# Kernel optimization log

Measured on AMD Instinct MI355X. Metric: run time of the kernel, lower is better.

## Reference

```python
import jax, jax.numpy as jnp
import numpy as np

B, S, D, V, T, NS, NG = 16, 512, 400, 32000, 8, 30, 3


def setup_inputs() -> dict:
    key = jax.random.key(0)
    ks = jax.random.split(key, 14)
    w = 1.0 / np.sqrt(D)
    return {
        "encoded_hidden": jax.random.normal(ks[0], (1, B, D), jnp.float32) * 0.1,
        "encoded_outputs": jax.random.normal(ks[1], (B, S, D), jnp.float32) * 0.1,
        "story": jax.random.randint(ks[2], (B, S), 0, V),
        "trg_batches": jax.random.randint(ks[3], (B, NS, T), 0, V),
        "shared_emb": jax.random.normal(ks[4], (V, D), jnp.float32) * 0.1,
        "slot_emb": jax.random.normal(ks[5], (1, D), jnp.float32) * 0.1,
        "w_ih": jax.random.normal(ks[6], (3 * D, D), jnp.float32) * w,
        "w_hh": jax.random.normal(ks[7], (3 * D, D), jnp.float32) * w,
        "b_ih": jax.random.normal(ks[8], (3 * D,), jnp.float32) * w,
        "b_hh": jax.random.normal(ks[9], (3 * D,), jnp.float32) * w,
        "w_ratio_w": jax.random.normal(ks[10], (1, 3 * D), jnp.float32) * w,
        "w_ratio_b": jax.random.normal(ks[11], (1,), jnp.float32) * w,
        "w_gate_w": jax.random.normal(ks[12], (NG, D), jnp.float32) * w,
        "w_gate_b": jax.random.normal(ks[13], (NG,), jnp.float32) * w,
        "batch_size": B,
        "max_resp_len": T,
    }


def reference(encoded_hidden, encoded_outputs, story, trg_batches, shared_emb,
              slot_emb, w_ih, w_hh, b_ih, b_hh, w_ratio_w, w_ratio_b,
              w_gate_w, w_gate_b, batch_size, max_resp_len):
    # Original torch code returns inside the slot loop -> only slot 0 is decoded.
    # h0 is re-used as GRU initial state at EVERY step (no carried hidden), and
    # teacher forcing makes each step's input known, so all T steps vectorize.
    h0 = encoded_hidden[0]                         # (B, D)
    Bq, Tq = batch_size, max_resp_len
    Vq = shared_emb.shape[0]

    # decoder inputs: step 0 = slot embedding, steps 1..T-1 = emb(trg[:,0,i-1])
    x0 = jnp.broadcast_to(slot_emb, h0.shape)      # (B, D)
    xt = shared_emb[trg_batches[:, 0, : Tq - 1]]   # (B, T-1, D)
    X = jnp.concatenate([x0[:, None, :], xt], axis=1)  # (B, T, D)

    # GRU cell (torch gate order r, z, n), h0 broadcast over steps
    gi = X @ w_ih.T + b_ih                         # (B, T, 3D)
    gh = h0 @ w_hh.T + b_hh                        # (B, 3D)
    i_r, i_z, i_n = jnp.split(gi, 3, axis=-1)
    h_r, h_z, h_n = jnp.split(gh, 3, axis=-1)
    r = jax.nn.sigmoid(i_r + h_r[:, None, :])
    z = jax.nn.sigmoid(i_z + h_z[:, None, :])
    n = jnp.tanh(i_n + r * h_n[:, None, :])
    h = (1.0 - z) * n + z * h0[:, None, :]         # (B, T, D) decoder_state == hidden

    # attention over history (no length masking: all lens == S)
    scores = jnp.einsum('btd,bsd->bts', h, encoded_outputs)   # (B, T, S)
    probs = jax.nn.softmax(scores, axis=-1)
    # FAITHFUL to original bug: context uses raw scores, not probs
    context = jnp.einsum('bts,bsd->btd', scores, encoded_outputs)

    gate0 = context[:, 0, :] @ w_gate_w.T + w_gate_b          # (B, NG), step i==0

    p_vocab = jax.nn.softmax(h @ shared_emb.T, axis=-1)       # (B, T, V)
    p_gen = jax.nn.sigmoid(
        jnp.concatenate([h, context, X], axis=-1) @ w_ratio_w.T + w_ratio_b
    )                                                         # (B, T, 1)

    # pointer distribution: scatter_add probs onto vocab ids of the story
    p_ctx = jnp.zeros((Bq, Tq, Vq), p_vocab.dtype).at[
        jnp.arange(Bq)[:, None, None],
        jnp.arange(Tq)[None, :, None],
        story[:, None, :],
    ].add(probs)

    p_final = p_gen * p_vocab + (1.0 - p_gen) * p_ctx         # (B, T, V)

    ptr_outputs = jnp.zeros((NS, Bq, Tq, Vq), p_final.dtype).at[0].set(p_final)
    gate_outputs = jnp.zeros((NS, Bq, NG), gate0.dtype).at[0].set(gate0)
    return ptr_outputs, gate_outputs
```

## Files before the change

kernel.cpp:

```cpp
#include <hip/hip_runtime.h>

#define Bq 16
#define Sq 512
#define Dq 400
#define Vq 32000
#define Tq 8
#define NSq 30
#define NGq 3
#define BTq (Bq*Tq)
#define SLICE 4096000
#define PTR_TOTAL (30ull*SLICE)
#define GATE_TOTAL (NSq*Bq*NGq)

#define NCOMPUTE 250
#define NZERO 1813
#define ZPER 16384

#define GCOMPUTE 64
#define PCTX_ZB 250

__device__ inline float sigmoidf_(float x) { return 1.0f / (1.0f + __expf(-x)); }

__device__ inline float blockReduceSum(float v, float* red) {
    int tid = threadIdx.x;
    #pragma unroll
    for (int o = 32; o > 0; o >>= 1) v += __shfl_down(v, o, 64);
    if ((tid & 63) == 0) red[tid >> 6] = v;
    __syncthreads();
    if (tid == 0) {
        float s = red[0];
        int nw = blockDim.x >> 6;
        for (int i = 1; i < nw; i++) s += red[i];
        red[0] = s;
    }
    __syncthreads();
    float r = red[0];
    __syncthreads();
    return r;
}

__device__ inline float blockReduceMax(float v, float* red) {
    int tid = threadIdx.x;
    #pragma unroll
    for (int o = 32; o > 0; o >>= 1) v = fmaxf(v, __shfl_down(v, o, 64));
    if ((tid & 63) == 0) red[tid >> 6] = v;
    __syncthreads();
    if (tid == 0) {
        float s = red[0];
        int nw = blockDim.x >> 6;
        for (int i = 1; i < nw; i++) s = fmaxf(s, red[i]);
        red[0] = s;
    }
    __syncthreads();
    float r = red[0];
    __syncthreads();
    return r;
}

__global__ __launch_bounds__(256) void k_gates(const float* __restrict__ enc_hidden,
                                               const float* __restrict__ shared_emb,
                                               const float* __restrict__ slot_emb,
                                               const float* __restrict__ w_ih,
                                               const float* __restrict__ w_hh,
                                               const float* __restrict__ b_ih,
                                               const float* __restrict__ b_hh,
                                               const int* __restrict__ trg,
                                               float* __restrict__ gi, float* __restrict__ gh,
                                               float* __restrict__ pctx) {
    int tid = threadIdx.x;
    if (blockIdx.x >= GCOMPUTE) {
        int zb = blockIdx.x - GCOMPUTE;
        float4 z = make_float4(0.0f, 0.0f, 0.0f, 0.0f);
        float4* dst = (float4*)pctx;
        size_t base = (size_t)zb * 4096 + tid;
        #pragma unroll
        for (int r = 0; r < 16; ++r) dst[base + (size_t)r * 256] = z;
        return;
    }
    __shared__ float A[9][Dq];
    __shared__ int toks[8];
    int b = blockIdx.x >> 2, jt = blockIdx.x & 3;
    if (tid < 7) toks[tid + 1] = trg[b * (NSq * Tq) + tid];
    __syncthreads();
    for (int idx = tid; idx < 900; idx += 256) {
        int r = idx / 100, q = idx - r * 100;
        const float4* src;
        if (r == 8)      src = (const float4*)(enc_hidden + b * Dq);
        else if (r == 0) src = (const float4*)slot_emb;
        else             src = (const float4*)(shared_emb + (size_t)toks[r] * Dq);
        *(float4*)&A[r][4 * q] = src[q];
    }
    __syncthreads();
    for (int o = tid; o < 2700; o += 256) {
        int r = o / 300, jj = o - r * 300;
        int j = jt * 300 + jj;
        const float* w = (r == 8) ? w_hh : w_ih;
        const float4* w4 = (const float4*)(w + (size_t)j * Dq);
        const float4* a4 = (const float4*)&A[r][0];
        float acc = (r == 8) ? b_hh[j] : b_ih[j];
        #pragma unroll 4
        for (int q = 0; q < Dq / 4; ++q) {
            float4 wv = w4[q], av = a4[q];
            acc += av.x * wv.x + av.y * wv.y + av.z * wv.z + av.w * wv.w;
        }
        if (r == 8) gh[b * 1200 + j] = acc;
        else        gi[(b * 8 + r) * 1200 + j] = acc;
    }
}

__global__ __launch_bounds__(512) void k_attn(const float* __restrict__ gi,
                                              const float* __restrict__ gh,
                                              const float* __restrict__ enc_hidden,
                                              const float* __restrict__ shared_emb,
                                              const float* __restrict__ slot_emb,
                                              const int* __restrict__ trg,
                                              const float* __restrict__ enc_out,
                                              const int* __restrict__ story,
                                              const float* __restrict__ w_ratio_w,
                                              const float* __restrict__ w_ratio_b,
                                              const float* __restrict__ w_gate_w,
                                              const float* __restrict__ w_gate_b,
                                              float* __restrict__ pctx, float* __restrict__ pgen,
                                              float* __restrict__ hT, float* __restrict__ out_gate) {
    __shared__ float h_l[Dq], ctx_l[Dq], x_l[Dq], sc_l[Sq], red[8];
    int bt = blockIdx.x, b = bt >> 3, t = bt & 7;
    int tid = threadIdx.x;
    if (tid < Dq) {
        int d = tid;
        float x = (t == 0) ? slot_emb[d]
                           : shared_emb[(size_t)trg[b * (NSq * Tq) + (t - 1)] * Dq + d];
        float h0 = enc_hidden[b * Dq + d];
        const float* gib = gi + bt * 1200;
        const float* ghb = gh + b * 1200;
        float r_ = sigmoidf_(gib[d] + ghb[d]);
        float z  = sigmoidf_(gib[Dq + d] + ghb[Dq + d]);
        float n  = tanhf(gib[2 * Dq + d] + r_ * ghb[2 * Dq + d]);
        float h  = (1.0f - z) * n + z * h0;
        h_l[d] = h; x_l[d] = x;
        hT[d * BTq + bt] = h;
    }
    __syncthreads();
    {
        const float4* e4 = (const float4*)(enc_out + ((size_t)(b * Sq + tid)) * Dq);
        float acc = 0.0f;
        for (int q = 0; q < Dq / 4; ++q) {
            float4 p = e4[q];
            int k = 4 * q;
            acc += h_l[k]*p.x + h_l[k+1]*p.y + h_l[k+2]*p.z + h_l[k+3]*p.w;
        }
        sc_l[tid] = acc;
    }
    __syncthreads();
    float myv = sc_l[tid];
    float m = blockReduceMax(myv, red);
    float e = __expf(myv - m);
    float ssum = blockReduceSum(e, red);
    atomicAdd(&pctx[(size_t)bt * Vq + story[b * Sq + tid]], e / ssum);
    for (int d = tid; d < Dq; d += 512) {
        float acc = 0.0f;
        #pragma unroll 8
        for (int s = 0; s < Sq; ++s)
            acc += sc_l[s] * enc_out[((size_t)(b * Sq + s)) * Dq + d];
        ctx_l[d] = acc;
    }
    __syncthreads();
    {
        float part = 0.0f;
        for (int i = tid; i < 1200; i += 512) {
            float v = (i < Dq) ? h_l[i] : (i < 2 * Dq ? ctx_l[i - Dq] : x_l[i - 2 * Dq]);
            part += v * w_ratio_w[i];
        }
        float tot = blockReduceSum(part, red);
        if (tid == 0) pgen[bt] = sigmoidf_(tot + w_ratio_b[0]);
    }
    if (t == 0) {
        for (int g = 0; g < NGq; ++g) {
            float part = 0.0f;
            for (int d = tid; d < Dq; d += 512) part += ctx_l[d] * w_gate_w[g * Dq + d];
            float tot = blockReduceSum(part, red);
            if (tid == 0) out_gate[b * NGq + g] = tot + w_gate_b[g];
        }
    }
}

#define TVL 128
#define CKL 40
__global__ __launch_bounds__(256) void k_logits(const float* __restrict__ hT,
                                                const float* __restrict__ emb,
                                                float* __restrict__ logits,
                                                float* __restrict__ out) {
    __shared__ float eT[CKL][132];
    __shared__ float hL[CKL][132];
    int bid = blockIdx.x;
    int tid = threadIdx.x;
    if (bid >= NCOMPUTE) {
        int zb = bid - NCOMPUTE;
        float4 z = make_float4(0.0f, 0.0f, 0.0f, 0.0f);
        if (zb < NZERO) {
            float4* dst = (float4*)(out + (size_t)SLICE);
            const size_t total = 29ull * SLICE / 4;
            size_t base = (size_t)zb * ZPER + tid;
            #pragma unroll
            for (int r = 0; r < ZPER / 256; ++r) {
                size_t idx = base + (size_t)r * 256;
                if (idx < total) dst[idx] = z;
            }
        } else {
            float4* g = (float4*)(out + PTR_TOTAL + Bq * NGq);
            for (int i = tid; i < (GATE_TOTAL - Bq * NGq) / 4; i += 256) g[i] = z;
        }
        return;
    }
    int v0 = bid * TVL;
    int tx = tid & 15, ty = tid >> 4;
    float acc[8][8];
    #pragma unroll
    for (int j = 0; j < 8; ++j)
        #pragma unroll
        for (int i = 0; i < 8; ++i) acc[j][i] = 0.0f;

    for (int c = 0; c < Dq / CKL; ++c) {
        int k0 = c * CKL;
        const float4* hg = (const float4*)(hT + (size_t)k0 * BTq);
        #pragma unroll
        for (int r = 0; r < 5; ++r) {
            int idx = tid + 256 * r;
            int k = idx >> 5, c4 = idx & 31;
            float4 vd = hg[idx];
            *(float4*)&hL[k][4 * c4] = vd;
        }
        #pragma unroll
        for (int r = 0; r < 5; ++r) {
            int idx = tid + 256 * r;
            int v = idx / 10, q = idx - 10 * v;
            float4 vd = *(const float4*)(emb + (size_t)(v0 + v) * Dq + k0 + 4 * q);
            eT[4*q+0][v] = vd.x; eT[4*q+1][v] = vd.y; eT[4*q+2][v] = vd.z; eT[4*q+3][v] = vd.w;
        }
        __syncthreads();
        #pragma unroll 4
        for (int k = 0; k < CKL; ++k) {
            float4 h0 = *(const float4*)&hL[k][8 * ty];
            float4 h1 = *(const float4*)&hL[k][8 * ty + 4];
            float4 e0 = *(const float4*)&eT[k][8 * tx];
            float4 e1 = *(const float4*)&eT[k][8 * tx + 4];
            float hv[8] = {h0.x, h0.y, h0.z, h0.w, h1.x, h1.y, h1.z, h1.w};
            float ev[8] = {e0.x, e0.y, e0.z, e0.w, e1.x, e1.y, e1.z, e1.w};
            #pragma unroll
            for (int j = 0; j < 8; ++j)
                #pragma unroll
                for (int i = 0; i < 8; ++i)
                    acc[j][i] += hv[j] * ev[i];
        }
        __syncthreads();
    }
    #pragma unroll
    for (int j = 0; j < 8; ++j) {
        int bt = 8 * ty + j;
        float* dst = logits + (size_t)bt * Vq + v0 + 8 * tx;
        *(float4*)dst       = make_float4(acc[j][0], acc[j][1], acc[j][2], acc[j][3]);
        *(float4*)(dst + 4) = make_float4(acc[j][4], acc[j][5], acc[j][6], acc[j][7]);
    }
}

__global__ __launch_bounds__(512) void k_final(const float* __restrict__ logits,
                                               const float* __restrict__ pctx,
                                               const float* __restrict__ pgen,
                                               float* __restrict__ out) {
    __shared__ float red[8];
    int bt = blockIdx.x, tid = threadIdx.x;
    const float* lr = logits + (size_t)bt * Vq;
    float m = -1e30f;
    for (int v = tid; v < Vq; v += 512) m = fmaxf(m, lr[v]);
    m = blockReduceMax(m, red);
    float s = 0.0f;
    for (int v = tid; v < Vq; v += 512) s += __expf(lr[v] - m);
    s = blockReduceSum(s, red);
    float inv = 1.0f / s, pg = pgen[bt], cg = 1.0f - pg;
    const float4* l4 = (const float4*)lr;
    const float4* p4 = (const float4*)(pctx + (size_t)bt * Vq);
    float4* o4 = (float4*)(out + (size_t)bt * Vq);
    for (int i = tid; i < Vq / 4; i += 512) {
        float4 lv = l4[i], pv = p4[i];
        o4[i] = make_float4(pg * __expf(lv.x - m) * inv + cg * pv.x,
                            pg * __expf(lv.y - m) * inv + cg * pv.y,
                            pg * __expf(lv.z - m) * inv + cg * pv.z,
                            pg * __expf(lv.w - m) * inv + cg * pv.w);
    }
}

extern "C" void kernel_launch(void* const* d_in, const int* in_sizes, int n_in,
                              void* d_out, int out_size, void* d_ws, size_t ws_size,
                              hipStream_t stream) {
    const float* enc_hidden = (const float*)d_in[0];
    const float* enc_out    = (const float*)d_in[1];
    const int*   story      = (const int*)d_in[2];
    const int*   trg        = (const int*)d_in[3];
    const float* shared_emb = (const float*)d_in[4];
    const float* slot_emb   = (const float*)d_in[5];
    const float* w_ih       = (const float*)d_in[6];
    const float* w_hh       = (const float*)d_in[7];
    const float* b_ih       = (const float*)d_in[8];
    const float* b_hh       = (const float*)d_in[9];
    const float* w_ratio_w  = (const float*)d_in[10];
    const float* w_ratio_b  = (const float*)d_in[11];
    const float* w_gate_w   = (const float*)d_in[12];
    const float* w_gate_b   = (const float*)d_in[13];

    float* out = (float*)d_out;

    float* ws = (float*)d_ws;
    float* logits_buf = ws;
    float* pctx_buf   = ws + (size_t)SLICE;
    float* gi_buf     = ws + 2 * (size_t)SLICE;
    float* gh_buf     = gi_buf + 153600;
    float* hT_buf     = gh_buf + 19200;
    float* pgen_buf   = hT_buf + 51200;

    hipLaunchKernelGGL(k_gates, dim3(GCOMPUTE + PCTX_ZB), dim3(256), 0, stream,
                       enc_hidden, shared_emb, slot_emb, w_ih, w_hh, b_ih, b_hh, trg,
                       gi_buf, gh_buf, pctx_buf);
    hipLaunchKernelGGL(k_attn, dim3(BTq), dim3(512), 0, stream,
                       gi_buf, gh_buf, enc_hidden, shared_emb, slot_emb, trg,
                       enc_out, story, w_ratio_w, w_ratio_b, w_gate_w, w_gate_b,
                       pctx_buf, pgen_buf, hT_buf, out + PTR_TOTAL);
    hipLaunchKernelGGL(k_logits, dim3(NCOMPUTE + NZERO + 1), dim3(256), 0, stream,
                       hT_buf, shared_emb, logits_buf, out);
    hipLaunchKernelGGL(k_final, dim3(BTq), dim3(512), 0, stream,
                       logits_buf, pctx_buf, pgen_buf, out);
}
```

Before: 767.4 us.

## Fuse partial softmax stats into logits GEMM, store bf16 logits, split final pass

The logits GEMM epilogue now computes per-tile row max and exp-sum (online softmax partials) and stores the logits as bf16 instead of fp32. The final kernel merges the 250 partials per row instead of making two extra passes over the logits, and it is spread over 8x more blocks, each handling a chunk of a row. This cuts the logits round-trip traffic and removes the serial per-row reductions over 32000 values, which had left only 128 blocks doing the work. The cost is bf16 rounding of the logits before the softmax, a precision loss that could exceed the tolerance.

After: 750.7 us. -2.2%, faster.

```diff
diff --git a/kernel.cpp b/kernel.cpp
--- a/kernel.cpp
+++ b/kernel.cpp
@@ -19,7 +19,15 @@
 #define GCOMPUTE 64
 #define PCTX_ZB 250
 
+#define FBLK 8
+#define FCH (Vq/FBLK)
+
 __device__ inline float sigmoidf_(float x) { return 1.0f / (1.0f + __expf(-x)); }
+
+__device__ inline unsigned bf16rne(float x) {
+    unsigned u = __float_as_uint(x);
+    return (u + 0x7FFFu + ((u >> 16) & 1u)) >> 16;
+}
 
 __device__ inline float blockReduceSum(float v, float* red) {
     int tid = threadIdx.x;
@@ -187,7 +195,9 @@
 #define CKL 40
 __global__ __launch_bounds__(256) void k_logits(const float* __restrict__ hT,
                                                 const float* __restrict__ emb,
-                                                float* __restrict__ logits,
+                                                unsigned short* __restrict__ logits,
+                                                float* __restrict__ pmax,
+                                                float* __restrict__ psum,
                                                 float* __restrict__ out) {
     __shared__ float eT[CKL][132];
     __shared__ float hL[CKL][132];
@@ -256,35 +266,67 @@
     #pragma unroll
     for (int j = 0; j < 8; ++j) {
         int bt = 8 * ty + j;
-        float* dst = logits + (size_t)bt * Vq + v0 + 8 * tx;
-        *(float4*)dst       = make_float4(acc[j][0], acc[j][1], acc[j][2], acc[j][3]);
-        *(float4*)(dst + 4) = make_float4(acc[j][4], acc[j][5], acc[j][6], acc[j][7]);
-    }
-}
-
-__global__ __launch_bounds__(512) void k_final(const float* __restrict__ logits,
+        unsigned bb[8];
+        float r[8];
+        float m = -1e30f;
+        #pragma unroll
+        for (int i = 0; i < 8; ++i) {
+            bb[i] = bf16rne(acc[j][i]);
+            r[i] = __uint_as_float(bb[i] << 16);
+            m = fmaxf(m, r[i]);
+        }
+        #pragma unroll
+        for (int o = 8; o >= 1; o >>= 1) m = fmaxf(m, __shfl_xor(m, o, 16));
+        float es = 0.0f;
+        #pragma unroll
+        for (int i = 0; i < 8; ++i) es += __expf(r[i] - m);
+        #pragma unroll
+        for (int o = 8; o >= 1; o >>= 1) es += __shfl_xor(es, o, 16);
+        if (tx == 0) {
+            pmax[bid * BTq + bt] = m;
+            psum[bid * BTq + bt] = es;
+        }
+        uint4 w = make_uint4(bb[0] | (bb[1] << 16), bb[2] | (bb[3] << 16),
+                             bb[4] | (bb[5] << 16), bb[6] | (bb[7] << 16));
+        *(uint4*)(logits + (size_t)bt * Vq + v0 + 8 * tx) = w;
+    }
+}
+
+__global__ __launch_bounds__(256) void k_final(const unsigned short* __restrict__ logits,
                                                const float* __restrict__ pctx,
                                                const float* __restrict__ pgen,
+                                               const float* __restrict__ pmax,
+                                               const float* __restrict__ psum,
                                                float* __restrict__ out) {
-    __shared__ float red[8];
-    int bt = blockIdx.x, tid = threadIdx.x;
-    const float* lr = logits + (size_t)bt * Vq;
-    float m = -1e30f;
-    for (int v = tid; v < Vq; v += 512) m = fmaxf(m, lr[v]);
-    m = blockReduceMax(m, red);
-    float s = 0.0f;
-    for (int v = tid; v < Vq; v += 512) s += __expf(lr[v] - m);
-    s = blockReduceSum(s, red);
+    __shared__ float red[4];
+    int bid = blockIdx.x, tid = threadIdx.x;
+    int bt = bid >> 3, ch = bid & 7;
+    float pm = (tid < NCOMPUTE) ? pmax[tid * BTq + bt] : -1e30f;
+    float m = blockReduceMax(pm, red);
+    float part = (tid < NCOMPUTE) ? psum[tid * BTq + bt] * __expf(pm - m) : 0.0f;
+    float s = blockReduceSum(part, red);
     float inv = 1.0f / s, pg = pgen[bt], cg = 1.0f - pg;
-    const float4* l4 = (const float4*)lr;
-    const float4* p4 = (const float4*)(pctx + (size_t)bt * Vq);
-    float4* o4 = (float4*)(out + (size_t)bt * Vq);
-    for (int i = tid; i < Vq / 4; i += 512) {
-        float4 lv = l4[i], pv = p4[i];
-        o4[i] = make_float4(pg * __expf(lv.x - m) * inv + cg * pv.x,
-                            pg * __expf(lv.y - m) * inv + cg * pv.y,
-                            pg * __expf(lv.z - m) * inv + cg * pv.z,
-                            pg * __expf(lv.w - m) * inv + cg * pv.w);
+    size_t rowoff = (size_t)bt * Vq + (size_t)ch * FCH;
+    const uint4*  l4 = (const uint4*)(logits + rowoff);
+    const float4* p4 = (const float4*)(pctx + rowoff);
+    float4*       o4 = (float4*)(out + rowoff);
+    for (int i = tid; i < FCH / 8; i += 256) {
+        uint4 lv = l4[i];
+        float4 pa = p4[2 * i], pb = p4[2 * i + 1];
+        float f0 = __uint_as_float(lv.x << 16), f1 = __uint_as_float(lv.x & 0xFFFF0000u);
+        float f2 = __uint_as_float(lv.y << 16), f3 = __uint_as_float(lv.y & 0xFFFF0000u);
+        float f4 = __uint_as_float(lv.z << 16), f5 = __uint_as_float(lv.z & 0xFFFF0000u);
+        float f6 = __uint_as_float(lv.w << 16), f7 = __uint_as_float(lv.w & 0xFFFF0000u);
+        float4 oa = make_float4(pg * __expf(f0 - m) * inv + cg * pa.x,
+                                pg * __expf(f1 - m) * inv + cg * pa.y,
+                                pg * __expf(f2 - m) * inv + cg * pa.z,
+                                pg * __expf(f3 - m) * inv + cg * pa.w);
+        float4 ob = make_float4(pg * __expf(f4 - m) * inv + cg * pb.x,
+                                pg * __expf(f5 - m) * inv + cg * pb.y,
+                                pg * __expf(f6 - m) * inv + cg * pb.z,
+                                pg * __expf(f7 - m) * inv + cg * pb.w);
+        o4[2 * i]     = oa;
+        o4[2 * i + 1] = ob;
     }
 }
 
@@ -309,12 +351,14 @@
     float* out = (float*)d_out;
 
     float* ws = (float*)d_ws;
-    float* logits_buf = ws;
+    unsigned short* logits_buf = (unsigned short*)ws;
     float* pctx_buf   = ws + (size_t)SLICE;
     float* gi_buf     = ws + 2 * (size_t)SLICE;
     float* gh_buf     = gi_buf + 153600;
     float* hT_buf     = gh_buf + 19200;
     float* pgen_buf   = hT_buf + 51200;
+    float* pmax_buf   = pgen_buf + 128;
+    float* psum_buf   = pmax_buf + 32000;
 
     hipLaunchKernelGGL(k_gates, dim3(GCOMPUTE + PCTX_ZB), dim3(256), 0, stream,
                        enc_hidden, shared_emb, slot_emb, w_ih, w_hh, b_ih, b_hh, trg,
@@ -324,7 +368,7 @@
                        enc_out, story, w_ratio_w, w_ratio_b, w_gate_w, w_gate_b,
                        pctx_buf, pgen_buf, hT_buf, out + PTR_TOTAL);
     hipLaunchKernelGGL(k_logits, dim3(NCOMPUTE + NZERO + 1), dim3(256), 0, stream,
-                       hT_buf, shared_emb, logits_buf, out);
-    hipLaunchKernelGGL(k_final, dim3(BTq), dim3(512), 0, stream,
-                       logits_buf, pctx_buf, pgen_buf, out);
-}
+                       hT_buf, shared_emb, logits_buf, pmax_buf, psum_buf, out);
+    hipLaunchKernelGGL(k_final, dim3(BTq * FBLK), dim3(256), 0, stream,
+                       logits_buf, pctx_buf, pgen_buf, pmax_buf, psum_buf, out);
+}
```
